# Optimization experiments

Hardware: AMD Instinct MI355X
Metric: run time of the kernel (lower is better)

The kernel has to match this reference:

```python
import jax, jax.numpy as jnp
from jax import lax
import numpy as np

# ITA requantization params (from init_kwargs)
MQ, SQ = 16384, 8
MK, SK = 16384, 8
MV, SV = 16384, 8
MA, SA = 5, 12
MAV, SAV = 1, 8
MO, SO = 256, 7
NUM_HEADS = 6


def requantize(x, mult, shift, add=0):
    # x * mult, floor-div by 2**shift, add, clamp to int8 range (values kept in float32)
    return jnp.clip(jnp.floor(x * mult / (2.0 ** shift)) + add, -128.0, 127.0)


def ita_softmax(x):
    # x: [B, h, S, Skv] float32 with integer values in [-128, 127]
    B, h, S, Skv = x.shape
    width, bits = 16, 8
    eps_max = 32.0 * bits / (2 ** bits)  # range_scale * bits / 2**bits = 1.0
    groups = Skv // width
    x3 = x.reshape(B * h, S, Skv).astype(jnp.int32)
    # [groups, BH, S, width] for streaming scan over key chunks
    chunks = x3.reshape(B * h, S, groups, width).transpose(2, 0, 1, 3)

    def step(carry, chunk):
        exp_partial_sum, global_max = carry
        current_max = chunk.max(axis=-1)
        update = current_max > global_max
        max_shift = jnp.floor((current_max - global_max).astype(jnp.float32) * eps_max + 0.5).astype(jnp.int32)
        shift_sum = jnp.where(update, max_shift, 0)
        global_max = jnp.where(update, current_max, global_max)
        diff = global_max[..., None] - chunk  # >= 0
        shift = jnp.floor(diff.astype(jnp.float32) * eps_max + 0.5).astype(jnp.int32)
        # 2**bits >> shift  (256 >> shift; any shift >= 9 yields 0, clamp to keep shift defined)
        exp_sum = jnp.sum(jnp.right_shift(jnp.int32(256), jnp.minimum(shift, 31)), axis=-1).astype(jnp.int32)
        exp_partial_sum = jnp.right_shift(exp_partial_sum, jnp.minimum(shift_sum, 31)) + exp_sum
        return (exp_partial_sum, global_max), None

    init = (jnp.zeros((B * h, S), jnp.int32), jnp.full((B * h, S), -128, jnp.int32))
    (exp_partial_sum, global_max), _ = lax.scan(step, init, chunks)

    # (2**bits - 1) * 2**bits = 65280
    inv = jnp.floor(65280.0 / exp_partial_sum.astype(jnp.float32)).astype(jnp.int32)
    diff = global_max[..., None] - x3  # >= 0
    shift = jnp.floor(diff.astype(jnp.float32) * eps_max + 0.5).astype(jnp.int32)
    res = jnp.right_shift(inv[..., None], jnp.minimum(shift, 31)).astype(jnp.uint8)
    return res.reshape(B, h, S, Skv)


def setup_inputs() -> dict:
    key = jax.random.key(0)
    ks = jax.random.split(key, 9)
    B, N, D = 4, 2048, 384
    scale = 1.0 / np.sqrt(D)
    return {
        "x": jax.random.normal(ks[0], (B, N, D), jnp.float32),
        "wq": jax.random.normal(ks[1], (D, D), jnp.float32) * scale,
        "bq": jnp.zeros((D,), jnp.float32),
        "wk": jax.random.normal(ks[2], (D, D), jnp.float32) * scale,
        "bk": jnp.zeros((D,), jnp.float32),
        "wv": jax.random.normal(ks[3], (D, D), jnp.float32) * scale,
        "bv": jnp.zeros((D,), jnp.float32),
        "wo": jax.random.normal(ks[4], (D, D), jnp.float32) * scale,
        "bo": jnp.zeros((D,), jnp.float32),
        "H": 64,
        "W": 32,
    }


def reference(x, wq, bq, wk, bk, wv, bv, wo, bo, H, W):
    B, N, _ = x.shape
    h = NUM_HEADS
    hd = wq.shape[0] // h

    Q = requantize(x @ wq.T + bq, MQ, SQ)
    K = requantize(x @ wk.T + bk, MK, SK)
    V = requantize(x @ wv.T + bv, MV, SV)

    Qr = Q.reshape(B, N, h, hd).transpose(0, 2, 1, 3)  # [B,h,N,hd]
    Kr = K.reshape(B, N, h, hd).transpose(0, 2, 1, 3)
    Vr = V.reshape(B, N, h, hd).transpose(0, 2, 1, 3)

    logits = requantize(jnp.einsum('bhqd,bhkd->bhqk', Qr, Kr), MA, SA)
    attn = ita_softmax(logits)  # uint8 [B,h,N,N]
    ctx = requantize(jnp.einsum('bhqk,bhkd->bhqd', attn.astype(jnp.float32), Vr), MAV, SAV)
    ctx = ctx.transpose(0, 2, 1, 3).reshape(B, N, h * hd)
    out = requantize(ctx @ wo.T + bo, MO, SO)
    return out
```

## Files before the change

### kernel.cpp

```cpp
#include <hip/hip_runtime.h>
#include <stdint.h>

#define NB 4
#define NN 2048
#define ND 384
#define NH 6
#define HD 64
#define ROWS (NB * NN)

typedef int v4i __attribute__((ext_vector_type(4)));

#if defined(__has_builtin)
#if __has_builtin(__builtin_amdgcn_sdot4)
#define HAVE_SDOT4 1
#endif
#endif

__device__ __forceinline__ int dot4i8(int a, int b, int c) {
#ifdef HAVE_SDOT4
    return __builtin_amdgcn_sdot4(a, b, c, false);
#else
    c += (int)(int8_t)(a & 0xFF) * (int)(int8_t)(b & 0xFF);
    c += (int)(int8_t)((a >> 8) & 0xFF) * (int)(int8_t)((b >> 8) & 0xFF);
    c += (int)(int8_t)((a >> 16) & 0xFF) * (int)(int8_t)((b >> 16) & 0xFF);
    c += (int)(int8_t)((a >> 24) & 0xFF) * (int)(int8_t)((b >> 24) & 0xFF);
    return c;
#endif
}

__global__ __launch_bounds__(256) void qkv_gemm_kernel(
    const float* __restrict__ X,
    const float* __restrict__ Wq, const float* __restrict__ Wk, const float* __restrict__ Wv,
    const float* __restrict__ Bq, const float* __restrict__ Bk, const float* __restrict__ Bv,
    int8_t* __restrict__ Q8, int8_t* __restrict__ K8, int8_t* __restrict__ V8T)
{
    __shared__ float As[16][68];
    __shared__ float Bs[16][68];

    const int t = threadIdx.x;
    const int row0 = blockIdx.x * 64;
    const int jb = blockIdx.y;
    const int m = jb / 6;
    const int c0 = (jb % 6) * 64;
    const float* W = (m == 0) ? Wq : (m == 1) ? Wk : Wv;
    const float* Bi = (m == 0) ? Bq : (m == 1) ? Bk : Bv;

    const int li = t >> 2;
    const int lk = (t & 3) << 2;
    const int tx = t & 15, ty = t >> 4;

    float acc[4][4] = {{0.f}};

    for (int k0 = 0; k0 < ND; k0 += 16) {
        float4 a = *(const float4*)&X[(size_t)(row0 + li) * ND + k0 + lk];
        float4 b = *(const float4*)&W[(size_t)(c0 + li) * ND + k0 + lk];
        As[lk + 0][li] = a.x; As[lk + 1][li] = a.y; As[lk + 2][li] = a.z; As[lk + 3][li] = a.w;
        Bs[lk + 0][li] = b.x; Bs[lk + 1][li] = b.y; Bs[lk + 2][li] = b.z; Bs[lk + 3][li] = b.w;
        __syncthreads();
#pragma unroll
        for (int kk = 0; kk < 16; kk++) {
            float4 av = *(const float4*)&As[kk][ty * 4];
            float4 bv = *(const float4*)&Bs[kk][tx * 4];
            float aa[4] = {av.x, av.y, av.z, av.w};
            float bb[4] = {bv.x, bv.y, bv.z, bv.w};
#pragma unroll
            for (int i = 0; i < 4; i++)
#pragma unroll
                for (int j = 0; j < 4; j++)
                    acc[i][j] += aa[i] * bb[j];
        }
        __syncthreads();
    }

    if (m == 2) {
        const int r0 = row0 + ty * 4;
        const int bidx = r0 >> 11;
        const int n0 = r0 & 2047;
#pragma unroll
        for (int j = 0; j < 4; j++) {
            const int c = c0 + tx * 4 + j;
            const int head = c >> 6, dim = c & 63;
            uint32_t w = 0;
#pragma unroll
            for (int i = 0; i < 4; i++) {
                float v = acc[i][j] + Bi[c];
                int qv = (int)floorf(v * 64.0f);
                qv = max(-128, min(127, qv));
                w |= (uint32_t)(qv & 255) << (8 * i);
            }
            *(uint32_t*)(V8T + (((size_t)(bidx * NH + head) * HD + dim) * NN + n0)) = w;
        }
    } else {
        int8_t* Out = (m == 0) ? Q8 : K8;
#pragma unroll
        for (int i = 0; i < 4; i++) {
            const int r = row0 + ty * 4 + i;
            const int bidx = r >> 11;
            const int n = r & 2047;
#pragma unroll
            for (int j = 0; j < 4; j++) {
                const int c = c0 + tx * 4 + j;
                float v = acc[i][j] + Bi[c];
                int qv = (int)floorf(v * 64.0f);
                qv = max(-128, min(127, qv));
                const int head = c >> 6, dim = c & 63;
                Out[(((size_t)(bidx * NH + head) * NN) + n) * HD + dim] = (int8_t)qv;
            }
        }
    }
}

__global__ __launch_bounds__(256) void colsum_kernel(
    const int8_t* __restrict__ V8T, int* __restrict__ colsum)
{
    __shared__ int part[256];
    const int bh = blockIdx.x;
    const int t = threadIdx.x;
    const int d = t >> 2, pp = t & 3;
    const int* p = (const int*)(V8T + (size_t)bh * NN * HD + (size_t)d * NN + pp * 512);
    int s = 0;
#pragma unroll 4
    for (int i = 0; i < 128; ++i) s = dot4i8(p[i], 0x01010101, s);
    part[t] = s;
    __syncthreads();
    if (pp == 0) colsum[bh * 64 + d] = part[t] + part[t + 1] + part[t + 2] + part[t + 3];
}

__global__ __launch_bounds__(256, 3) void attn_kernel(
    const int8_t* __restrict__ Q8, const int8_t* __restrict__ K8,
    const int8_t* __restrict__ V8T, const int* __restrict__ colsum,
    int8_t* __restrict__ CTX8)
{
    __shared__ int Lp[128 * 68];
    __shared__ int stats[2 * 16 * 132];
    __shared__ int invq[16];
    __shared__ int gmq[16];

    int* gmax = stats;
    int* esum = stats + 16 * 132;

    const int t = threadIdx.x;
    const int wid = t >> 6;
    const int lane = t & 63;
    const int quad = lane >> 4;
    const int l15 = lane & 15;
    const int bh = blockIdx.y;
    const int q0 = blockIdx.x * 16;
    const size_t base = (size_t)bh * NN * HD;
    const v4i zero = {0, 0, 0, 0};

    v4i afrag = *(const v4i*)(Q8 + base + (size_t)(q0 + l15) * HD + quad * 16);
    for (int kt = wid * 32; kt < wid * 32 + 32; ++kt) {
        v4i bfrag = *(const v4i*)(K8 + base + (size_t)(kt * 16 + l15) * HD + quad * 16);
        v4i d = __builtin_amdgcn_mfma_i32_16x16x64_i8(afrag, bfrag, zero, 0, 0, 0);
        int w = 0;
#pragma unroll
        for (int r = 0; r < 4; ++r) {
            int lg = (d[r] * 5) >> 12;
            lg = min(127, max(-128, lg));
            w |= (lg & 255) << (8 * r);
        }
        Lp[kt * 68 + quad * 16 + l15] = w;
    }
    __syncthreads();

#pragma unroll
    for (int it = 0; it < 2; ++it) {
        const int task = t + it * 256;
        const int g = task & 127, qq = task >> 7;
        const int* p = &Lp[g * 68 + qq * 16];
        int wb[16];
#pragma unroll
        for (int a = 0; a < 4; ++a) {
            v4i v = *(const v4i*)&p[a * 4];
            wb[a * 4 + 0] = v.x; wb[a * 4 + 1] = v.y; wb[a * 4 + 2] = v.z; wb[a * 4 + 3] = v.w;
        }
#pragma unroll
        for (int b = 0; b < 4; ++b) {
            int mx = INT_MIN;
#pragma unroll
            for (int j = 0; j < 16; ++j)
                mx = max(mx, (int)((unsigned)wb[j] << (8 * (3 - b))));
            gmax[(qq * 4 + b) * 132 + g] = (mx >> 24);
        }
    }
    __syncthreads();

    if (t < 16) {
        int m = -128;
        for (int g4 = 0; g4 < 128; g4 += 4) {
            v4i v = *(v4i*)&gmax[t * 132 + g4];
            m = max(m, v.x); v.x = m;
            m = max(m, v.y); v.y = m;
            m = max(m, v.z); v.z = m;
            m = max(m, v.w); v.w = m;
            *(v4i*)&gmax[t * 132 + g4] = v;
        }
    }
    __syncthreads();

#pragma unroll
    for (int it = 0; it < 2; ++it) {
        const int task = t + it * 256;
        const int g = task & 127, qq = task >> 7;
        const int* p = &Lp[g * 68 + qq * 16];
        int wb[16];
#pragma unroll
        for (int a = 0; a < 4; ++a) {
            v4i v = *(const v4i*)&p[a * 4];
            wb[a * 4 + 0] = v.x; wb[a * 4 + 1] = v.y; wb[a * 4 + 2] = v.z; wb[a * 4 + 3] = v.w;
        }
#pragma unroll
        for (int b = 0; b < 4; ++b) {
            const int M = gmax[(qq * 4 + b) * 132 + g];
            const int cb = 8 - M;
            int s = 0;
#pragma unroll
            for (int j = 0; j < 16; ++j) {
                int x = (int)(int8_t)(wb[j] >> (8 * b));
                int tt = x + cb;
                s += (tt >= 0) ? (1 << tt) : 0;
            }
            esum[(qq * 4 + b) * 132 + g] = s;
        }
    }
    __syncthreads();

    if (t < 16) {
        int E = 0, Mp = -128;
        for (int g = 0; g < 128; ++g) {
            int m = gmax[t * 132 + g];
            int d = m - Mp; if (d > 31) d = 31;
            E = (E >> d) + esum[t * 132 + g];
            Mp = m;
        }
        invq[t] = 65280 / E;
        gmq[t] = Mp;
    }
    __syncthreads();

    {
        const int qw = t & 3;
        const int k15 = (t >> 2) & 15;
        const int band = t >> 6;
        int c24[4]; unsigned invv[4];
#pragma unroll
        for (int b = 0; b < 4; ++b) {
            c24[b] = 24 - gmq[qw * 4 + b];
            invv[b] = (unsigned)invq[qw * 4 + b];
        }
        for (int j = 0; j < 32; ++j) {
            const int kt = band * 32 + j;
            const int idx = kt * 68 + qw * 16 + k15;
            const int w = Lp[idx];
            unsigned outw = 0;
#pragma unroll
            for (int b = 0; b < 4; ++b) {
                int x = (int)(int8_t)(w >> (8 * b));
                int t1 = x + c24[b];
                t1 = (t1 < 0) ? 0 : t1;
                unsigned a = (invv[b] << t1) >> 24;
                outw |= ((a - 128u) & 255u) << (8 * b);
            }
            Lp[idx] = (int)outw;
        }
    }
    __syncthreads();

    const int sh8 = 8 * (l15 & 3);
    v4i accs[4] = {zero, zero, zero, zero};
    const int8_t* vtb = V8T + base;

    for (int kc = wid * 8; kc < wid * 8 + 8; ++kc) {
        const int* lp = &Lp[(kc * 4 + quad) * 68 + (l15 >> 2) * 16];
        v4i a;
#pragma unroll
        for (int r = 0; r < 4; ++r) {
            const int w0 = lp[4 * r + 0], w1 = lp[4 * r + 1];
            const int w2 = lp[4 * r + 2], w3 = lp[4 * r + 3];
            a[r] = (int)((((unsigned)w0 >> sh8) & 255u) |
                         ((((unsigned)w1 >> sh8) & 255u) << 8) |
                         ((((unsigned)w2 >> sh8) & 255u) << 16) |
                         ((((unsigned)w3 >> sh8) & 255u) << 24));
        }
        const int koff = kc * 64 + quad * 16;
        v4i b0 = *(const v4i*)(vtb + (size_t)(0 * 16 + l15) * NN + koff);
        v4i b1 = *(const v4i*)(vtb + (size_t)(1 * 16 + l15) * NN + koff);
        v4i b2 = *(const v4i*)(vtb + (size_t)(2 * 16 + l15) * NN + koff);
        v4i b3 = *(const v4i*)(vtb + (size_t)(3 * 16 + l15) * NN + koff);
        accs[0] = __builtin_amdgcn_mfma_i32_16x16x64_i8(a, b0, accs[0], 0, 0, 0);
        accs[1] = __builtin_amdgcn_mfma_i32_16x16x64_i8(a, b1, accs[1], 0, 0, 0);
        accs[2] = __builtin_amdgcn_mfma_i32_16x16x64_i8(a, b2, accs[2], 0, 0, 0);
        accs[3] = __builtin_amdgcn_mfma_i32_16x16x64_i8(a, b3, accs[3], 0, 0, 0);
    }
    __syncthreads();

    if (wid > 0) {
#pragma unroll
        for (int dt = 0; dt < 4; ++dt)
#pragma unroll
            for (int r = 0; r < 4; ++r)
                stats[(dt * 4 + r) * 192 + (wid - 1) * 64 + lane] = accs[dt][r];
    }
    __syncthreads();
    if (wid == 0) {
        const int bb = bh / NH, hh = bh % NH;
        const int* cs = &colsum[bh * 64];
#pragma unroll
        for (int dt = 0; dt < 4; ++dt) {
            const int dcol = dt * 16 + l15;
            const int corr = cs[dcol] << 7;
#pragma unroll
            for (int r = 0; r < 4; ++r) {
                const int i = dt * 4 + r;
                int val = accs[dt][r]
                        + stats[i * 192 + 0 * 64 + lane]
                        + stats[i * 192 + 1 * 64 + lane]
                        + stats[i * 192 + 2 * 64 + lane];
                const int q = q0 + quad * 4 + r;
                val = (val + corr) >> 8;
                val = min(127, max(-128, val));
                CTX8[((size_t)(bb * NN + q)) * ND + hh * HD + dcol] = (int8_t)val;
            }
        }
    }
}

__global__ __launch_bounds__(256) void out_gemm_kernel(
    const int8_t* __restrict__ CTX8, const float* __restrict__ Wo,
    const float* __restrict__ Bo, float* __restrict__ out)
{
    __shared__ float As[16][68];
    __shared__ float Bs[16][68];

    const int t = threadIdx.x;
    const int row0 = blockIdx.x * 64;
    const int c0 = blockIdx.y * 64;
    const int li = t >> 2;
    const int lk = (t & 3) << 2;
    const int tx = t & 15, ty = t >> 4;

    float acc[4][4] = {{0.f}};

    for (int k0 = 0; k0 < ND; k0 += 16) {
        const int av = *(const int*)&CTX8[(size_t)(row0 + li) * ND + k0 + lk];
        float4 b = *(const float4*)&Wo[(size_t)(c0 + li) * ND + k0 + lk];
        As[lk + 0][li] = (float)(int)(int8_t)(av & 0xFF);
        As[lk + 1][li] = (float)(int)(int8_t)((av >> 8) & 0xFF);
        As[lk + 2][li] = (float)(int)(int8_t)((av >> 16) & 0xFF);
        As[lk + 3][li] = (float)(int)(int8_t)((av >> 24) & 0xFF);
        Bs[lk + 0][li] = b.x; Bs[lk + 1][li] = b.y; Bs[lk + 2][li] = b.z; Bs[lk + 3][li] = b.w;
        __syncthreads();
#pragma unroll
        for (int kk = 0; kk < 16; kk++) {
            float4 avv = *(const float4*)&As[kk][ty * 4];
            float4 bvv = *(const float4*)&Bs[kk][tx * 4];
            float aa[4] = {avv.x, avv.y, avv.z, avv.w};
            float bb[4] = {bvv.x, bvv.y, bvv.z, bvv.w};
#pragma unroll
            for (int i = 0; i < 4; i++)
#pragma unroll
                for (int j = 0; j < 4; j++)
                    acc[i][j] += aa[i] * bb[j];
        }
        __syncthreads();
    }

#pragma unroll
    for (int i = 0; i < 4; i++) {
        const int r = row0 + ty * 4 + i;
#pragma unroll
        for (int j = 0; j < 4; j++) {
            const int c = c0 + tx * 4 + j;
            float v = acc[i][j] + Bo[c];
            float rq = floorf(v * 2.0f);
            rq = fminf(fmaxf(rq, -128.0f), 127.0f);
            out[(size_t)r * ND + c] = rq;
        }
    }
}

extern "C" void kernel_launch(void* const* d_in, const int* in_sizes, int n_in,
                              void* d_out, int out_size, void* d_ws, size_t ws_size,
                              hipStream_t stream)
{
    const float* x  = (const float*)d_in[0];
    const float* wq = (const float*)d_in[1];
    const float* bq = (const float*)d_in[2];
    const float* wk = (const float*)d_in[3];
    const float* bk = (const float*)d_in[4];
    const float* wv = (const float*)d_in[5];
    const float* bv = (const float*)d_in[6];
    const float* wo = (const float*)d_in[7];
    const float* bo = (const float*)d_in[8];
    float* out = (float*)d_out;

    const size_t MAT = (size_t)ROWS * ND;
    int8_t* Q8  = (int8_t*)d_ws;
    int8_t* K8  = Q8 + MAT;
    int8_t* V8T = K8 + MAT;
    int8_t* C8  = V8T + MAT;
    int*    CS  = (int*)(C8 + MAT);

    qkv_gemm_kernel<<<dim3(ROWS / 64, 18), 256, 0, stream>>>(
        x, wq, wk, wv, bq, bk, bv, Q8, K8, V8T);
    colsum_kernel<<<dim3(NB * NH), 256, 0, stream>>>(V8T, CS);
    attn_kernel<<<dim3(NN / 16, NB * NH), 256, 0, stream>>>(Q8, K8, V8T, CS, C8);
    out_gemm_kernel<<<dim3(ROWS / 64, ND / 64), 256, 0, stream>>>(C8, wo, bo, out);
}
```

Before: 315.1 us.

## Use 128x128 register tiles in projection GEMMs and fuse V column sums

Both fp32 projection GEMMs move from 64x64 tiles with 4x4 per-thread outputs to 128x128 tiles with 8x8 per-thread outputs. This raises arithmetic intensity per shared-memory load and halves the number of tiles. The V-column sum is now computed in the QKV GEMM epilogue with shared-memory and global atomics, which removes the separate colsum kernel but adds a memset launch. The risks are higher register pressure from 64 accumulators and fewer blocks: 576 for QKV and only 192 for the output GEMM, which may underfill the GPU.

```diff
diff --git a/kernel.cpp b/kernel.cpp
--- a/kernel.cpp
+++ b/kernel.cpp
@@ -10,96 +10,105 @@
 
 typedef int v4i __attribute__((ext_vector_type(4)));
 
-#if defined(__has_builtin)
-#if __has_builtin(__builtin_amdgcn_sdot4)
-#define HAVE_SDOT4 1
-#endif
-#endif
-
-__device__ __forceinline__ int dot4i8(int a, int b, int c) {
-#ifdef HAVE_SDOT4
-    return __builtin_amdgcn_sdot4(a, b, c, false);
-#else
-    c += (int)(int8_t)(a & 0xFF) * (int)(int8_t)(b & 0xFF);
-    c += (int)(int8_t)((a >> 8) & 0xFF) * (int)(int8_t)((b >> 8) & 0xFF);
-    c += (int)(int8_t)((a >> 16) & 0xFF) * (int)(int8_t)((b >> 16) & 0xFF);
-    c += (int)(int8_t)((a >> 24) & 0xFF) * (int)(int8_t)((b >> 24) & 0xFF);
-    return c;
-#endif
-}
-
 __global__ __launch_bounds__(256) void qkv_gemm_kernel(
     const float* __restrict__ X,
     const float* __restrict__ Wq, const float* __restrict__ Wk, const float* __restrict__ Wv,
     const float* __restrict__ Bq, const float* __restrict__ Bk, const float* __restrict__ Bv,
-    int8_t* __restrict__ Q8, int8_t* __restrict__ K8, int8_t* __restrict__ V8T)
+    int8_t* __restrict__ Q8, int8_t* __restrict__ K8, int8_t* __restrict__ V8T,
+    int* __restrict__ CS)
 {
-    __shared__ float As[16][68];
-    __shared__ float Bs[16][68];
+    __shared__ float As[16][132];
+    __shared__ float Bs[16][132];
+    __shared__ int lcol[128];
 
     const int t = threadIdx.x;
-    const int row0 = blockIdx.x * 64;
-    const int jb = blockIdx.y;
-    const int m = jb / 6;
-    const int c0 = (jb % 6) * 64;
+    const int row0 = blockIdx.x * 128;
+    const int c0g = blockIdx.y * 128;
+    const int m = c0g / ND;
+    const int cl0 = c0g - m * ND;
     const float* W = (m == 0) ? Wq : (m == 1) ? Wk : Wv;
     const float* Bi = (m == 0) ? Bq : (m == 1) ? Bk : Bv;
 
-    const int li = t >> 2;
-    const int lk = (t & 3) << 2;
-    const int tx = t & 15, ty = t >> 4;
-
-    float acc[4][4] = {{0.f}};
+    const int tx = t & 15;
+    const int ty = t >> 4;
+    const int lr = t >> 1;
+    const int kh = (t & 1) * 8;
+
+    float acc[8][8];
+#pragma unroll
+    for (int i = 0; i < 8; i++)
+#pragma unroll
+        for (int j = 0; j < 8; j++) acc[i][j] = 0.f;
+
+    const float* xrow = X + (size_t)(row0 + lr) * ND + kh;
+    const float* wrow = W + (size_t)(cl0 + lr) * ND + kh;
 
     for (int k0 = 0; k0 < ND; k0 += 16) {
-        float4 a = *(const float4*)&X[(size_t)(row0 + li) * ND + k0 + lk];
-        float4 b = *(const float4*)&W[(size_t)(c0 + li) * ND + k0 + lk];
-        As[lk + 0][li] = a.x; As[lk + 1][li] = a.y; As[lk + 2][li] = a.z; As[lk + 3][li] = a.w;
-        Bs[lk + 0][li] = b.x; Bs[lk + 1][li] = b.y; Bs[lk + 2][li] = b.z; Bs[lk + 3][li] = b.w;
+        float4 a0 = *(const float4*)(xrow + k0);
+        float4 a1 = *(const float4*)(xrow + k0 + 4);
+        float4 b0 = *(const float4*)(wrow + k0);
+        float4 b1 = *(const float4*)(wrow + k0 + 4);
+        As[kh + 0][lr] = a0.x; As[kh + 1][lr] = a0.y; As[kh + 2][lr] = a0.z; As[kh + 3][lr] = a0.w;
+        As[kh + 4][lr] = a1.x; As[kh + 5][lr] = a1.y; As[kh + 6][lr] = a1.z; As[kh + 7][lr] = a1.w;
+        Bs[kh + 0][lr] = b0.x; Bs[kh + 1][lr] = b0.y; Bs[kh + 2][lr] = b0.z; Bs[kh + 3][lr] = b0.w;
+        Bs[kh + 4][lr] = b1.x; Bs[kh + 5][lr] = b1.y; Bs[kh + 6][lr] = b1.z; Bs[kh + 7][lr] = b1.w;
         __syncthreads();
 #pragma unroll
         for (int kk = 0; kk < 16; kk++) {
-            float4 av = *(const float4*)&As[kk][ty * 4];
-            float4 bv = *(const float4*)&Bs[kk][tx * 4];
-            float aa[4] = {av.x, av.y, av.z, av.w};
-            float bb[4] = {bv.x, bv.y, bv.z, bv.w};
-#pragma unroll
-            for (int i = 0; i < 4; i++)
-#pragma unroll
-                for (int j = 0; j < 4; j++)
-                    acc[i][j] += aa[i] * bb[j];
-        }
-        __syncthreads();
-    }
-
+            float a[8], b[8];
+#pragma unroll
+            for (int i = 0; i < 8; i++) a[i] = As[kk][ty * 8 + i];
+#pragma unroll
+            for (int j = 0; j < 8; j++) b[j] = Bs[kk][tx + 16 * j];
+#pragma unroll
+            for (int i = 0; i < 8; i++)
+#pragma unroll
+                for (int j = 0; j < 8; j++)
+                    acc[i][j] += a[i] * b[j];
+        }
+        __syncthreads();
+    }
+
+    const int bidx = row0 >> 11;
     if (m == 2) {
-        const int r0 = row0 + ty * 4;
-        const int bidx = r0 >> 11;
-        const int n0 = r0 & 2047;
-#pragma unroll
-        for (int j = 0; j < 4; j++) {
-            const int c = c0 + tx * 4 + j;
+        if (t < 128) lcol[t] = 0;
+        __syncthreads();
+        const int n0 = row0 & 2047;
+#pragma unroll
+        for (int j = 0; j < 8; j++) {
+            const int c = cl0 + tx + 16 * j;
             const int head = c >> 6, dim = c & 63;
-            uint32_t w = 0;
-#pragma unroll
-            for (int i = 0; i < 4; i++) {
-                float v = acc[i][j] + Bi[c];
+            const float bias = Bi[c];
+            int s = 0;
+            uint32_t w[2] = {0u, 0u};
+#pragma unroll
+            for (int i = 0; i < 8; i++) {
+                float v = acc[i][j] + bias;
                 int qv = (int)floorf(v * 64.0f);
                 qv = max(-128, min(127, qv));
-                w |= (uint32_t)(qv & 255) << (8 * i);
+                s += qv;
+                w[i >> 2] |= (uint32_t)(qv & 255) << (8 * (i & 3));
             }
-            *(uint32_t*)(V8T + (((size_t)(bidx * NH + head) * HD + dim) * NN + n0)) = w;
+            uint32_t* dst = (uint32_t*)(V8T + (((size_t)(bidx * NH + head) * HD + dim) * NN
+                                              + n0 + ty * 8));
+            dst[0] = w[0];
+            dst[1] = w[1];
+            atomicAdd(&lcol[tx + 16 * j], s);
+        }
+        __syncthreads();
+        if (t < 128) {
+            const int c = cl0 + t;
+            atomicAdd(&CS[(bidx * NH + (c >> 6)) * 64 + (c & 63)], lcol[t]);
         }
     } else {
         int8_t* Out = (m == 0) ? Q8 : K8;
 #pragma unroll
-        for (int i = 0; i < 4; i++) {
-            const int r = row0 + ty * 4 + i;
-            const int bidx = r >> 11;
+        for (int i = 0; i < 8; i++) {
+            const int r = row0 + ty * 8 + i;
             const int n = r & 2047;
 #pragma unroll
-            for (int j = 0; j < 4; j++) {
-                const int c = c0 + tx * 4 + j;
+            for (int j = 0; j < 8; j++) {
+                const int c = cl0 + tx + 16 * j;
                 float v = acc[i][j] + Bi[c];
                 int qv = (int)floorf(v * 64.0f);
                 qv = max(-128, min(127, qv));
@@ -108,22 +117,6 @@
             }
         }
     }
-}
-
-__global__ __launch_bounds__(256) void colsum_kernel(
-    const int8_t* __restrict__ V8T, int* __restrict__ colsum)
-{
-    __shared__ int part[256];
-    const int bh = blockIdx.x;
-    const int t = threadIdx.x;
-    const int d = t >> 2, pp = t & 3;
-    const int* p = (const int*)(V8T + (size_t)bh * NN * HD + (size_t)d * NN + pp * 512);
-    int s = 0;
-#pragma unroll 4
-    for (int i = 0; i < 128; ++i) s = dot4i8(p[i], 0x01010101, s);
-    part[t] = s;
-    __syncthreads();
-    if (pp == 0) colsum[bh * 64 + d] = part[t] + part[t + 1] + part[t + 2] + part[t + 3];
 }
 
 __global__ __launch_bounds__(256, 3) void attn_kernel(
@@ -330,48 +323,60 @@
     const int8_t* __restrict__ CTX8, const float* __restrict__ Wo,
     const float* __restrict__ Bo, float* __restrict__ out)
 {
-    __shared__ float As[16][68];
-    __shared__ float Bs[16][68];
+    __shared__ float As[16][132];
+    __shared__ float Bs[16][132];
 
     const int t = threadIdx.x;
-    const int row0 = blockIdx.x * 64;
-    const int c0 = blockIdx.y * 64;
-    const int li = t >> 2;
-    const int lk = (t & 3) << 2;
-    const int tx = t & 15, ty = t >> 4;
-
-    float acc[4][4] = {{0.f}};
+    const int row0 = blockIdx.x * 128;
+    const int c0 = blockIdx.y * 128;
+    const int tx = t & 15;
+    const int ty = t >> 4;
+    const int lr = t >> 1;
+    const int kh = (t & 1) * 8;
+
+    float acc[8][8];
+#pragma unroll
+    for (int i = 0; i < 8; i++)
+#pragma unroll
+        for (int j = 0; j < 8; j++) acc[i][j] = 0.f;
+
+    const int8_t* arow = CTX8 + (size_t)(row0 + lr) * ND + kh;
+    const float* wrow = Wo + (size_t)(c0 + lr) * ND + kh;
 
     for (int k0 = 0; k0 < ND; k0 += 16) {
-        const int av = *(const int*)&CTX8[(size_t)(row0 + li) * ND + k0 + lk];
-        float4 b = *(const float4*)&Wo[(size_t)(c0 + li) * ND + k0 + lk];
-        As[lk + 0][li] = (float)(int)(int8_t)(av & 0xFF);
-        As[lk + 1][li] = (float)(int)(int8_t)((av >> 8) & 0xFF);
-        As[lk + 2][li] = (float)(int)(int8_t)((av >> 16) & 0xFF);
-        As[lk + 3][li] = (float)(int)(int8_t)((av >> 24) & 0xFF);
-        Bs[lk + 0][li] = b.x; Bs[lk + 1][li] = b.y; Bs[lk + 2][li] = b.z; Bs[lk + 3][li] = b.w;
+        int2 a8 = *(const int2*)(arow + k0);
+        float4 b0 = *(const float4*)(wrow + k0);
+        float4 b1 = *(const float4*)(wrow + k0 + 4);
+#pragma unroll
+        for (int u = 0; u < 4; u++) {
+            As[kh + u][lr]     = (float)(int)(int8_t)((a8.x >> (8 * u)) & 0xFF);
+            As[kh + 4 + u][lr] = (float)(int)(int8_t)((a8.y >> (8 * u)) & 0xFF);
+        }
+        Bs[kh + 0][lr] = b0.x; Bs[kh + 1][lr] = b0.y; Bs[kh + 2][lr] = b0.z; Bs[kh + 3][lr] = b0.w;
+        Bs[kh + 4][lr] = b1.x; Bs[kh + 5][lr] = b1.y; Bs[kh + 6][lr] = b1.z; Bs[kh + 7][lr] = b1.w;
         __syncthreads();
 #pragma unroll
         for (int kk = 0; kk < 16; kk++) {
-            float4 avv = *(const float4*)&As[kk][ty * 4];
-            float4 bvv = *(const float4*)&Bs[kk][tx * 4];
-            float aa[4] = {avv.x, avv.y, avv.z, avv.w};
-            float bb[4] = {bvv.x, bvv.y, bvv.z, bvv.w};
-#pragma unroll
-            for (int i = 0; i < 4; i++)
-#pragma unroll
-                for (int j = 0; j < 4; j++)
-                    acc[i][j] += aa[i] * bb[j];
-        }
-        __syncthreads();
-    }
-
-#pragma unroll
-    for (int i = 0; i < 4; i++) {
-        const int r = row0 + ty * 4 + i;
-#pragma unroll
-        for (int j = 0; j < 4; j++) {
-            const int c = c0 + tx * 4 + j;
+            float a[8], b[8];
+#pragma unroll
+            for (int i = 0; i < 8; i++) a[i] = As[kk][ty * 8 + i];
+#pragma unroll
+            for (int j = 0; j < 8; j++) b[j] = Bs[kk][tx + 16 * j];
+#pragma unroll
+            for (int i = 0; i < 8; i++)
+#pragma unroll
+                for (int j = 0; j < 8; j++)
+                    acc[i][j] += a[i] * b[j];
+        }
+        __syncthreads();
+    }
+
+#pragma unroll
+    for (int i = 0; i < 8; i++) {
+        const int r = row0 + ty * 8 + i;
+#pragma unroll
+        for (int j = 0; j < 8; j++) {
+            const int c = c0 + tx + 16 * j;
             float v = acc[i][j] + Bo[c];
             float rq = floorf(v * 2.0f);
             rq = fminf(fmaxf(rq, -128.0f), 127.0f);
@@ -402,9 +407,9 @@
     int8_t* C8  = V8T + MAT;
     int*    CS  = (int*)(C8 + MAT);
 
-    qkv_gemm_kernel<<<dim3(ROWS / 64, 18), 256, 0, stream>>>(
-        x, wq, wk, wv, bq, bk, bv, Q8, K8, V8T);
-    colsum_kernel<<<dim3(NB * NH), 256, 0, stream>>>(V8T, CS);
+    hipMemsetAsync(CS, 0, (size_t)NB * NH * 64 * sizeof(int), stream);
+    qkv_gemm_kernel<<<dim3(ROWS / 128, 1152 / 128), 256, 0, stream>>>(
+        x, wq, wk, wv, bq, bk, bv, Q8, K8, V8T, CS);
     attn_kernel<<<dim3(NN / 16, NB * NH), 256, 0, stream>>>(Q8, K8, V8T, CS, C8);
-    out_gemm_kernel<<<dim3(ROWS / 64, ND / 64), 256, 0, stream>>>(C8, wo, bo, out);
+    out_gemm_kernel<<<dim3(ROWS / 128, ND / 128), 256, 0, stream>>>(C8, wo, bo, out);
 }
```

New measurement: 370.3 us. 1.18x slower.
